# Performance work log

Measured on AMD Instinct MI355X. Metric: run time of the kernel, lower is better.

The kernel has to match this reference:

```python
import jax, jax.numpy as jnp
import numpy as np

HIDDEN_DIM = 1024
NUM_HEADS = 16
HEAD_DIM = HIDDEN_DIM // NUM_HEADS


def setup_inputs() -> dict:
    key = jax.random.key(0)
    k1, k2, k3 = jax.random.split(key, 3)
    B, S, D = 2, 2048, HIDDEN_DIM
    x = jax.random.normal(k1, (B, S, D), dtype=jnp.float32)
    attention_mask = jnp.ones((B, S), dtype=jnp.int32)
    scale = 1.0 / np.sqrt(D)
    W_qkv = jax.random.normal(k2, (D, 3 * D), dtype=jnp.float32) * scale
    b_qkv = jnp.zeros((3 * D,), dtype=jnp.float32)
    W_out = jax.random.normal(k3, (D, D), dtype=jnp.float32) * scale
    b_out = jnp.zeros((D,), dtype=jnp.float32)
    return {"x": x, "attention_mask": attention_mask,
            "W_qkv": W_qkv, "b_qkv": b_qkv, "W_out": W_out, "b_out": b_out}


def reference(x, attention_mask, W_qkv, b_qkv, W_out, b_out):
    B, S, D = x.shape
    H, hd = NUM_HEADS, HEAD_DIM
    qkv = x @ W_qkv + b_qkv                     # [B,S,3D]
    # Faithful to torch: view to [B,S,H,3*hd] THEN chunk last dim (per-head interleaving)
    qkv = qkv.reshape(B, S, H, 3 * hd)
    q, k, v = jnp.split(qkv, 3, axis=-1)        # each [B,S,H,hd]
    scores = jnp.einsum('bqhd,bkhd->bhqk', q, k) / np.sqrt(hd)  # [B,H,S,S]
    mask = attention_mask[:, None, None, :]     # broadcast over heads, queries
    scores = jnp.where(mask == 0, -jnp.inf, scores)
    weights = jax.nn.softmax(scores, axis=-1)
    out = jnp.einsum('bhqk,bkhd->bqhd', weights, v).reshape(B, S, D)
    return out @ W_out + b_out
```

## Files before the change

kernel.cpp:

```cpp
#include <hip/hip_runtime.h>

#define SDIM 2048
#define NHEADS 16
#define HD 64

typedef __attribute__((ext_vector_type(8))) short bf16x8;
typedef __attribute__((ext_vector_type(8))) unsigned short u16x8;
typedef __attribute__((ext_vector_type(4))) float f32x4;
typedef unsigned short u16;

static __device__ __forceinline__ u16 f2bf(float f) {
  unsigned u = __builtin_bit_cast(unsigned, f);
  u += 0x7fffu + ((u >> 16) & 1u);
  return (u16)(u >> 16);
}

static __device__ __forceinline__ unsigned cvt_pk_bf16(float lo, float hi) {
  unsigned r;
  asm("v_cvt_pk_bf16_f32 %0, %1, %2" : "=v"(r) : "v"(lo), "v"(hi));
  return r;
}

static __device__ __forceinline__ f32x4 mfma16(bf16x8 a, bf16x8 b, f32x4 c) {
  return __builtin_amdgcn_mfma_f32_16x16x32_bf16(a, b, c, 0, 0, 0);
}

static __device__ __forceinline__ void gload16(const u16* g, u16* l) {
  __builtin_amdgcn_global_load_lds(
      (const __attribute__((address_space(1))) void*)g,
      (__attribute__((address_space(3))) void*)l, 16, 0, 0);
}

__global__ void cvt_kernel(const float* __restrict__ in, u16* __restrict__ out, int n8) {
  int i = blockIdx.x * blockDim.x + threadIdx.x;
  if (i >= n8) return;
  const float4* p = (const float4*)(in + (long)i * 8);
  float4 a = p[0], b = p[1];
  u16x8 r;
  r[0] = f2bf(a.x); r[1] = f2bf(a.y); r[2] = f2bf(a.z); r[3] = f2bf(a.w);
  r[4] = f2bf(b.x); r[5] = f2bf(b.y); r[6] = f2bf(b.z); r[7] = f2bf(b.w);
  *(u16x8*)(out + (long)i * 8) = r;
}

__global__ void transpose_cvt(const float* __restrict__ W, u16* __restrict__ Wt, int K, int N) {
  __shared__ float t[32][33];
  int tx = threadIdx.x & 31, ty = threadIdx.x >> 5;
  int n0 = blockIdx.x * 32, k0 = blockIdx.y * 32;
#pragma unroll
  for (int i = 0; i < 32; i += 8) t[ty + i][tx] = W[(long)(k0 + ty + i) * N + n0 + tx];
  __syncthreads();
#pragma unroll
  for (int i = 0; i < 32; i += 8) Wt[(long)(n0 + ty + i) * K + k0 + tx] = f2bf(t[tx][ty + i]);
}

__global__ __launch_bounds__(256) void vtrans_kernel(const u16* __restrict__ QKV,
                                                     u16* __restrict__ Vt) {
  __shared__ u16 t[64][72];
  const int bh = blockIdx.y, s0 = blockIdx.x * 64;
  const int b = bh >> 4, h = bh & 15;
  const u16* src = QKV + ((long)(b * SDIM + s0)) * 3072 + h * 192 + 128;
  int r = threadIdx.x >> 3, c = (threadIdx.x & 7) * 8;
  *(uint4*)&t[r][c]      = *(const uint4*)(src + (long)r * 3072 + c);
  *(uint4*)&t[r + 32][c] = *(const uint4*)(src + (long)(r + 32) * 3072 + c);
  __syncthreads();
  int d = threadIdx.x >> 2, sc = (threadIdx.x & 3) * 16;
  u16 tmp[16];
#pragma unroll
  for (int k = 0; k < 16; ++k) tmp[k] = t[sc + k][d];
  u16* dst = Vt + ((long)(bh * HD + d)) * SDIM + s0 + sc;
  *(uint4*)dst = *(uint4*)&tmp[0];
  *(uint4*)(dst + 8) = *(uint4*)&tmp[8];
}

template <int EPI>
__global__ __launch_bounds__(256) void gemm_bf16(
    const u16* __restrict__ A, const u16* __restrict__ Bt,
    const float* __restrict__ bias, float* __restrict__ Cf, u16* __restrict__ Cb,
    int M, int N, int K)
{
  __shared__ __align__(16) u16 As[128 * 64];
  __shared__ __align__(16) u16 Bs[128 * 64];
  const int tid = threadIdx.x, lane = tid & 63, wid = tid >> 6;
  const int wm = wid >> 1, wn = wid & 1;
  const int l15 = lane & 15, l4 = lane >> 4;
  const int m0 = blockIdx.y * 128, n0 = blockIdx.x * 128;
  const int srow = lane >> 3;
  const int schunk = (lane & 7) ^ srow;

  f32x4 acc[4][4];
#pragma unroll
  for (int i = 0; i < 4; ++i)
#pragma unroll
    for (int j = 0; j < 4; ++j) acc[i][j] = {0.f, 0.f, 0.f, 0.f};

  const int nk = K >> 6;
  for (int kt = 0; kt < nk; ++kt) {
    const int kc = kt << 6;
#pragma unroll
    for (int is = 0; is < 4; ++is) {
      int rb = wid * 32 + is * 8;
      int r = rb + srow;
      gload16(A  + (long)(m0 + r) * K + kc + schunk * 8, &As[rb * 64]);
      gload16(Bt + (long)(n0 + r) * K + kc + schunk * 8, &Bs[rb * 64]);
    }
    asm volatile("s_waitcnt vmcnt(0)" ::: "memory");
    __syncthreads();
#pragma unroll
    for (int kk = 0; kk < 2; ++kk) {
      bf16x8 af[4], bfr[4];
#pragma unroll
      for (int mt = 0; mt < 4; ++mt) {
        int row = wm * 64 + mt * 16 + l15;
        af[mt] = *(const bf16x8*)&As[row * 64 + (((kk * 4 + l4) ^ (l15 & 7)) * 8)];
      }
#pragma unroll
      for (int nt = 0; nt < 4; ++nt) {
        int row = wn * 64 + nt * 16 + l15;
        bfr[nt] = *(const bf16x8*)&Bs[row * 64 + (((kk * 4 + l4) ^ (l15 & 7)) * 8)];
      }
#pragma unroll
      for (int mt = 0; mt < 4; ++mt)
#pragma unroll
        for (int nt = 0; nt < 4; ++nt)
          acc[mt][nt] = mfma16(af[mt], bfr[nt], acc[mt][nt]);
    }
    __syncthreads();
  }

#pragma unroll
  for (int mt = 0; mt < 4; ++mt)
#pragma unroll
    for (int nt = 0; nt < 4; ++nt)
#pragma unroll
      for (int r = 0; r < 4; ++r) {
        int row = m0 + wm * 64 + mt * 16 + l4 * 4 + r;
        int col = n0 + wn * 64 + nt * 16 + l15;
        float v = acc[mt][nt][r] + bias[col];
        if (EPI == 0) Cf[(long)row * N + col] = v;
        else          Cb[(long)row * N + col] = f2bf(v);
      }
}

__global__ __launch_bounds__(512) void attn_kernel(
    const u16* __restrict__ QKV, const u16* __restrict__ Vtg,
    const int* __restrict__ maskg, u16* __restrict__ Og)
{
  __shared__ __align__(16) u16 Ks[2][64][64];
  __shared__ __align__(16) u16 Vs[2][64][64];
  __shared__ __align__(16) u16 Ps[128][64];
  const int tid = threadIdx.x, lane = tid & 63, w = tid >> 6;
  const int l15 = lane & 15, l4 = lane >> 4;
  const int bh = blockIdx.y, qt = blockIdx.x;
  const int b = bh >> 4, h = bh & 15;
  const u16* Qp = QKV + ((long)(b * SDIM + qt * 128)) * 3072 + h * 192;
  const u16* Kp = QKV + (long)(b * SDIM) * 3072 + h * 192 + 64;
  const u16* Vp = Vtg + (long)bh * HD * SDIM;
  const int* mp = maskg + b * SDIM;
  const float SC = 0.18033688011112042f;

  bf16x8 qa[2];
#pragma unroll
  for (int ks = 0; ks < 2; ++ks)
    qa[ks] = *(const bf16x8*)(Qp + (long)(w * 16 + l15) * 3072 + ks * 32 + l4 * 8);

  f32x4 O[4];
  float lsum[4];
#pragma unroll
  for (int dt = 0; dt < 4; ++dt) O[dt] = {0.f, 0.f, 0.f, 0.f};
#pragma unroll
  for (int r = 0; r < 4; ++r) lsum[r] = 0.f;

  char* KsB = (char*)&Ks[0][0][0];
  char* VsB = (char*)&Vs[0][0][0];
  char* PsB = (char*)&Ps[0][0];
  const int srow = lane >> 3;
  const int schunk = (lane & 7) ^ srow;

  auto stage = [&](int kt2, int buf) {
    int row = w * 8 + srow;
    gload16(Kp + (long)(kt2 * 64 + row) * 3072 + schunk * 8,
            (u16*)(KsB + buf * 8192 + (w * 8) * 128));
    gload16(Vp + (long)row * SDIM + kt2 * 64 + schunk * 8,
            (u16*)(VsB + buf * 8192 + (w * 8) * 128));
  };

  stage(0, 0);
  asm volatile("s_waitcnt vmcnt(0)" ::: "memory");
  __syncthreads();

  for (int kt = 0; kt < SDIM / 64; ++kt) {
    const int cur = kt & 1;
    if (kt + 1 < SDIM / 64) stage(kt + 1, cur ^ 1);

    float mbM[4];
#pragma unroll
    for (int nt = 0; nt < 4; ++nt)
      mbM[nt] = (mp[kt * 64 + nt * 16 + l15] ? 0.f : -1e30f) - 12.0f;

    f32x4 sc4[4];
    __builtin_amdgcn_s_setprio(1);
#pragma unroll
    for (int nt = 0; nt < 4; ++nt) {
      const char* krow = KsB + cur * 8192 + (nt * 16 + l15) * 128;
      bf16x8 kb0 = *(const bf16x8*)(krow + (((0 + l4) ^ (l15 & 7)) << 4));
      bf16x8 kb1 = *(const bf16x8*)(krow + (((4 + l4) ^ (l15 & 7)) << 4));
      f32x4 z = {0.f, 0.f, 0.f, 0.f};
      z = mfma16(qa[0], kb0, z);
      z = mfma16(qa[1], kb1, z);
      sc4[nt] = z;
    }
    __builtin_amdgcn_s_setprio(0);

#pragma unroll
    for (int r = 0; r < 4; ++r) {
      float p0 = __builtin_amdgcn_exp2f(sc4[0][r] * SC + mbM[0]);
      float p1 = __builtin_amdgcn_exp2f(sc4[1][r] * SC + mbM[1]);
      float p2 = __builtin_amdgcn_exp2f(sc4[2][r] * SC + mbM[2]);
      float p3 = __builtin_amdgcn_exp2f(sc4[3][r] * SC + mbM[3]);
      lsum[r] += (p0 + p1) + (p2 + p3);
      unsigned u01 = cvt_pk_bf16(p0, p1);
      unsigned u23 = cvt_pk_bf16(p2, p3);
      int prow = w * 16 + l4 * 4 + r;
      char* rb = PsB + prow * 128;
      int rx = prow & 7, bo = (l15 & 7) * 2, ch = l15 >> 3;
      *(u16*)(rb + (((0 + ch) ^ rx) << 4) + bo) = (u16)u01;
      *(u16*)(rb + (((2 + ch) ^ rx) << 4) + bo) = (u16)(u01 >> 16);
      *(u16*)(rb + (((4 + ch) ^ rx) << 4) + bo) = (u16)u23;
      *(u16*)(rb + (((6 + ch) ^ rx) << 4) + bo) = (u16)(u23 >> 16);
    }
    asm volatile("s_waitcnt lgkmcnt(0)" ::: "memory");
    __builtin_amdgcn_sched_barrier(0);

    __builtin_amdgcn_s_setprio(1);
#pragma unroll
    for (int ks2 = 0; ks2 < 2; ++ks2) {
      bf16x8 pa = *(const bf16x8*)(PsB + (w * 16 + l15) * 128 + (((ks2 * 4 + l4) ^ (l15 & 7)) << 4));
#pragma unroll
      for (int dt = 0; dt < 4; ++dt) {
        const char* vrow = VsB + cur * 8192 + (dt * 16 + l15) * 128;
        bf16x8 vb = *(const bf16x8*)(vrow + (((ks2 * 4 + l4) ^ (l15 & 7)) << 4));
        O[dt] = mfma16(pa, vb, O[dt]);
      }
    }
    __builtin_amdgcn_s_setprio(0);
    __syncthreads();
  }

  float inv[4];
#pragma unroll
  for (int r = 0; r < 4; ++r) {
    float s = lsum[r];
#pragma unroll
    for (int off = 1; off < 16; off <<= 1) s += __shfl_xor(s, off);
    inv[r] = 1.0f / s;
  }

#pragma unroll
  for (int dt = 0; dt < 4; ++dt)
#pragma unroll
    for (int r = 0; r < 4; ++r) {
      int s = qt * 128 + w * 16 + l4 * 4 + r;
      int d = dt * 16 + l15;
      Og[((long)(b * SDIM + s)) * 1024 + h * HD + d] = f2bf(O[dt][r] * inv[r]);
    }
}

extern "C" void kernel_launch(void* const* d_in, const int* in_sizes, int n_in,
                              void* d_out, int out_size, void* d_ws, size_t ws_size,
                              hipStream_t stream) {
  const float* x    = (const float*)d_in[0];
  const int*   am   = (const int*)d_in[1];
  const float* Wqkv = (const float*)d_in[2];
  const float* bqkv = (const float*)d_in[3];
  const float* Wout = (const float*)d_in[4];
  const float* bout = (const float*)d_in[5];
  float* out = (float*)d_out;
  char* ws = (char*)d_ws;

  u16* xb   = (u16*)(ws);
  u16* AOb  = (u16*)(ws);
  u16* wqt  = (u16*)(ws + (size_t) 8 * 1024 * 1024);
  u16* wot  = (u16*)(ws + (size_t)14 * 1024 * 1024);
  u16* QKVb = (u16*)(ws + (size_t)16 * 1024 * 1024);
  u16* Vtb  = (u16*)(ws + (size_t)40 * 1024 * 1024);

  cvt_kernel<<<2048, 256, 0, stream>>>(x, xb, 524288);
  transpose_cvt<<<dim3(96, 32), 256, 0, stream>>>(Wqkv, wqt, 1024, 3072);
  transpose_cvt<<<dim3(32, 32), 256, 0, stream>>>(Wout, wot, 1024, 1024);
  gemm_bf16<1><<<dim3(24, 32), 256, 0, stream>>>(xb, wqt, bqkv, nullptr, QKVb,
                                                 4096, 3072, 1024);
  vtrans_kernel<<<dim3(32, 32), 256, 0, stream>>>(QKVb, Vtb);
  attn_kernel<<<dim3(16, 32), 512, 0, stream>>>(QKVb, Vtb, am, AOb);
  gemm_bf16<0><<<dim3(8, 32), 256, 0, stream>>>(AOb, wot, bout, out, nullptr,
                                                4096, 1024, 1024);
}
```

Before: 141.4 us.

## Remap blocks across XCDs and precompute LDS offsets in attention loop

Switches the GEMM and attention launches to 1D grids and remaps block indices so that consecutive logical tiles land on the same XCD (blocks are dispatched round-robin over 8 XCDs). The goal is better L2 reuse of shared A/B tiles and of K/V for the same head. The attention kernel also precomputes swizzled LDS offsets and uses incrementing global pointers, which cuts per-iteration address arithmetic at the cost of more live registers.

```diff
diff --git a/kernel.cpp b/kernel.cpp
--- a/kernel.cpp
+++ b/kernel.cpp
@@ -83,7 +83,10 @@
   const int tid = threadIdx.x, lane = tid & 63, wid = tid >> 6;
   const int wm = wid >> 1, wn = wid & 1;
   const int l15 = lane & 15, l4 = lane >> 4;
-  const int m0 = blockIdx.y * 128, n0 = blockIdx.x * 128;
+  const int nblk = gridDim.x;
+  const int lb = (blockIdx.x & 7) * (nblk >> 3) + (blockIdx.x >> 3);
+  const int nx = N >> 7;
+  const int m0 = (lb / nx) * 128, n0 = (lb % nx) * 128;
   const int srow = lane >> 3;
   const int schunk = (lane & 7) ^ srow;
 
@@ -150,13 +153,14 @@
   __shared__ __align__(16) u16 Ps[128][64];
   const int tid = threadIdx.x, lane = tid & 63, w = tid >> 6;
   const int l15 = lane & 15, l4 = lane >> 4;
-  const int bh = blockIdx.y, qt = blockIdx.x;
+  const int lb = (blockIdx.x & 7) * 64 + (blockIdx.x >> 3);
+  const int qt = lb & 15, bh = lb >> 4;
   const int b = bh >> 4, h = bh & 15;
   const u16* Qp = QKV + ((long)(b * SDIM + qt * 128)) * 3072 + h * 192;
   const u16* Kp = QKV + (long)(b * SDIM) * 3072 + h * 192 + 64;
   const u16* Vp = Vtg + (long)bh * HD * SDIM;
-  const int* mp = maskg + b * SDIM;
   const float SC = 0.18033688011112042f;
+  const int NT = SDIM / 64;
 
   bf16x8 qa[2];
 #pragma unroll
@@ -176,34 +180,58 @@
   const int srow = lane >> 3;
   const int schunk = (lane & 7) ^ srow;
 
-  auto stage = [&](int kt2, int buf) {
-    int row = w * 8 + srow;
-    gload16(Kp + (long)(kt2 * 64 + row) * 3072 + schunk * 8,
-            (u16*)(KsB + buf * 8192 + (w * 8) * 128));
-    gload16(Vp + (long)row * SDIM + kt2 * 64 + schunk * 8,
-            (u16*)(VsB + buf * 8192 + (w * 8) * 128));
-  };
-
-  stage(0, 0);
+  u16* kDst[2] = { (u16*)(KsB + w * 1024), (u16*)(KsB + 8192 + w * 1024) };
+  u16* vDst[2] = { (u16*)(VsB + w * 1024), (u16*)(VsB + 8192 + w * 1024) };
+  const u16* kS = Kp + (long)(w * 8 + srow) * 3072 + schunk * 8;
+  const u16* vS = Vp + (long)(w * 8 + srow) * SDIM + schunk * 8;
+  const int* mrow = maskg + b * SDIM + l15;
+
+  int off[2][4];
+#pragma unroll
+  for (int j = 0; j < 2; ++j)
+#pragma unroll
+    for (int x = 0; x < 4; ++x)
+      off[j][x] = (x * 16 + l15) * 128 + (((j * 4 + l4) ^ (l15 & 7)) << 4);
+  int poffr[2];
+#pragma unroll
+  for (int j = 0; j < 2; ++j)
+    poffr[j] = (w * 16 + l15) * 128 + (((j * 4 + l4) ^ (l15 & 7)) << 4);
+  int pw[4][4];
+#pragma unroll
+  for (int r = 0; r < 4; ++r) {
+    int prow = w * 16 + l4 * 4 + r, rx = prow & 7, ch = l15 >> 3;
+    int rbase = prow * 128 + (l15 & 7) * 2;
+#pragma unroll
+    for (int c = 0; c < 4; ++c) pw[r][c] = rbase + (((2 * c + ch) ^ rx) << 4);
+  }
+
+  gload16(kS, kDst[0]); gload16(vS, vDst[0]);
+  kS += 64 * 3072; vS += 64;
   asm volatile("s_waitcnt vmcnt(0)" ::: "memory");
   __syncthreads();
 
-  for (int kt = 0; kt < SDIM / 64; ++kt) {
+  for (int kt = 0; kt < NT; ++kt) {
     const int cur = kt & 1;
-    if (kt + 1 < SDIM / 64) stage(kt + 1, cur ^ 1);
+    if (kt + 1 < NT) {
+      gload16(kS, kDst[cur ^ 1]); gload16(vS, vDst[cur ^ 1]);
+      kS += 64 * 3072; vS += 64;
+    }
 
     float mbM[4];
 #pragma unroll
     for (int nt = 0; nt < 4; ++nt)
-      mbM[nt] = (mp[kt * 64 + nt * 16 + l15] ? 0.f : -1e30f) - 12.0f;
+      mbM[nt] = (mrow[nt * 16] ? 0.f : -1e30f) - 12.0f;
+    mrow += 64;
+
+    const char* Kc = KsB + cur * 8192;
+    const char* Vc = VsB + cur * 8192;
 
     f32x4 sc4[4];
     __builtin_amdgcn_s_setprio(1);
 #pragma unroll
     for (int nt = 0; nt < 4; ++nt) {
-      const char* krow = KsB + cur * 8192 + (nt * 16 + l15) * 128;
-      bf16x8 kb0 = *(const bf16x8*)(krow + (((0 + l4) ^ (l15 & 7)) << 4));
-      bf16x8 kb1 = *(const bf16x8*)(krow + (((4 + l4) ^ (l15 & 7)) << 4));
+      bf16x8 kb0 = *(const bf16x8*)(Kc + off[0][nt]);
+      bf16x8 kb1 = *(const bf16x8*)(Kc + off[1][nt]);
       f32x4 z = {0.f, 0.f, 0.f, 0.f};
       z = mfma16(qa[0], kb0, z);
       z = mfma16(qa[1], kb1, z);
@@ -220,13 +248,10 @@
       lsum[r] += (p0 + p1) + (p2 + p3);
       unsigned u01 = cvt_pk_bf16(p0, p1);
       unsigned u23 = cvt_pk_bf16(p2, p3);
-      int prow = w * 16 + l4 * 4 + r;
-      char* rb = PsB + prow * 128;
-      int rx = prow & 7, bo = (l15 & 7) * 2, ch = l15 >> 3;
-      *(u16*)(rb + (((0 + ch) ^ rx) << 4) + bo) = (u16)u01;
-      *(u16*)(rb + (((2 + ch) ^ rx) << 4) + bo) = (u16)(u01 >> 16);
-      *(u16*)(rb + (((4 + ch) ^ rx) << 4) + bo) = (u16)u23;
-      *(u16*)(rb + (((6 + ch) ^ rx) << 4) + bo) = (u16)(u23 >> 16);
+      *(u16*)(PsB + pw[r][0]) = (u16)u01;
+      *(u16*)(PsB + pw[r][1]) = (u16)(u01 >> 16);
+      *(u16*)(PsB + pw[r][2]) = (u16)u23;
+      *(u16*)(PsB + pw[r][3]) = (u16)(u23 >> 16);
     }
     asm volatile("s_waitcnt lgkmcnt(0)" ::: "memory");
     __builtin_amdgcn_sched_barrier(0);
@@ -234,11 +259,10 @@
     __builtin_amdgcn_s_setprio(1);
 #pragma unroll
     for (int ks2 = 0; ks2 < 2; ++ks2) {
-      bf16x8 pa = *(const bf16x8*)(PsB + (w * 16 + l15) * 128 + (((ks2 * 4 + l4) ^ (l15 & 7)) << 4));
+      bf16x8 pa = *(const bf16x8*)(PsB + poffr[ks2]);
 #pragma unroll
       for (int dt = 0; dt < 4; ++dt) {
-        const char* vrow = VsB + cur * 8192 + (dt * 16 + l15) * 128;
-        bf16x8 vb = *(const bf16x8*)(vrow + (((ks2 * 4 + l4) ^ (l15 & 7)) << 4));
+        bf16x8 vb = *(const bf16x8*)(Vc + off[ks2][dt]);
         O[dt] = mfma16(pa, vb, O[dt]);
       }
     }
@@ -251,7 +275,7 @@
   for (int r = 0; r < 4; ++r) {
     float s = lsum[r];
 #pragma unroll
-    for (int off = 1; off < 16; off <<= 1) s += __shfl_xor(s, off);
+    for (int off2 = 1; off2 < 16; off2 <<= 1) s += __shfl_xor(s, off2);
     inv[r] = 1.0f / s;
   }
 
@@ -287,10 +311,10 @@
   cvt_kernel<<<2048, 256, 0, stream>>>(x, xb, 524288);
   transpose_cvt<<<dim3(96, 32), 256, 0, stream>>>(Wqkv, wqt, 1024, 3072);
   transpose_cvt<<<dim3(32, 32), 256, 0, stream>>>(Wout, wot, 1024, 1024);
-  gemm_bf16<1><<<dim3(24, 32), 256, 0, stream>>>(xb, wqt, bqkv, nullptr, QKVb,
-                                                 4096, 3072, 1024);
+  gemm_bf16<1><<<768, 256, 0, stream>>>(xb, wqt, bqkv, nullptr, QKVb,
+                                        4096, 3072, 1024);
   vtrans_kernel<<<dim3(32, 32), 256, 0, stream>>>(QKVb, Vtb);
-  attn_kernel<<<dim3(16, 32), 512, 0, stream>>>(QKVb, Vtb, am, AOb);
-  gemm_bf16<0><<<dim3(8, 32), 256, 0, stream>>>(AOb, wot, bout, out, nullptr,
-                                                4096, 1024, 1024);
-}
+  attn_kernel<<<512, 512, 0, stream>>>(QKVb, Vtb, am, AOb);
+  gemm_bf16<0><<<256, 256, 0, stream>>>(AOb, wot, bout, out, nullptr,
+                                        4096, 1024, 1024);
+}
```

Result: slower. 144.5 us (+2.2%).
